# Optimization experiments

Hardware: AMD Instinct MI355X
Metric: run time of the kernel (lower is better)

## Reference

```python
import jax, jax.numpy as jnp
import numpy as np

N_EMBD = 384
NUM_HEADS = 6
HEAD_SIZE = 64


def setup_inputs() -> dict:
    key = jax.random.key(0)
    ks = jax.random.split(key, 6)
    B, T = 128, 256
    D = NUM_HEADS * HEAD_SIZE  # 384
    x = jax.random.normal(ks[0], (B, T, N_EMBD), dtype=jnp.float32)
    Wk = jax.random.normal(ks[1], (N_EMBD, D), dtype=jnp.float32) * (N_EMBD ** -0.5)
    Wq = jax.random.normal(ks[2], (N_EMBD, D), dtype=jnp.float32) * (N_EMBD ** -0.5)
    Wv = jax.random.normal(ks[3], (N_EMBD, D), dtype=jnp.float32) * (N_EMBD ** -0.5)
    Wp = jax.random.normal(ks[4], (D, N_EMBD), dtype=jnp.float32) * (D ** -0.5)
    bp = jax.random.normal(ks[5], (N_EMBD,), dtype=jnp.float32) * 0.01
    return {"x": x, "Wk": Wk, "Wq": Wq, "Wv": Wv, "Wp": Wp, "bp": bp}


def reference(x, Wk, Wq, Wv, Wp, bp):
    B, T, C = x.shape
    H, hs = NUM_HEADS, HEAD_SIZE
    # QKV projections -> [B, H, T, hs]
    q = (x @ Wq).reshape(B, T, H, hs).transpose(0, 2, 1, 3)
    k = (x @ Wk).reshape(B, T, H, hs).transpose(0, 2, 1, 3)
    v = (x @ Wv).reshape(B, T, H, hs).transpose(0, 2, 1, 3)
    # NOTE: original scales by C**-0.5 where C = n_embd (not head_size)
    scale = jnp.asarray(C, x.dtype) ** -0.5
    wei = jnp.einsum('bhtd,bhsd->bhts', q, k) * scale  # [B, H, T, T]
    causal = jnp.tril(jnp.ones((T, T), dtype=bool))
    wei = jnp.where(causal, wei, -jnp.inf)
    wei = jax.nn.softmax(wei, axis=-1)
    # dropout disabled (eval mode) for deterministic reference
    out = jnp.einsum('bhts,bhsd->bhtd', wei, v)  # [B, H, T, hs]
    out = out.transpose(0, 2, 1, 3).reshape(B, T, H * hs)
    return out @ Wp + bp
```

## Files before the change

kernel.cpp:

```cpp
#include <hip/hip_runtime.h>
#include <hip/hip_bf16.h>


#define T_SEQ 256
#define NH 6
#define HS 64
#define CIN 384
#define BATCH 128
#define BT (BATCH * T_SEQ)
#define ELEMS ((size_t)BT * CIN)

using f32x4  = __attribute__((ext_vector_type(4))) float;
using bf16x8 = __attribute__((ext_vector_type(8))) short;

typedef __attribute__((address_space(3))) void       lds_vp;
typedef __attribute__((address_space(1))) const void glob_vp;

static __device__ __forceinline__ unsigned short f2bf(float f) {
  union { float f; unsigned u; } v; v.f = f;
  unsigned r = v.u + 0x7FFFu + ((v.u >> 16) & 1u);
  return (unsigned short)(r >> 16);
}

static __device__ __forceinline__ bf16x8 ld_bf8(const unsigned short* p) {
  return *reinterpret_cast<const bf16x8*>(p);
}

static __device__ __forceinline__ void gl_lds16(const void* g, void* l) {
  __builtin_amdgcn_global_load_lds((glob_vp*)g, (lds_vp*)l, 16, 0, 0);
}

__global__ __launch_bounds__(256) void convert_x(
    const float* __restrict__ x, unsigned short* __restrict__ xb)
{
  size_t i = (((size_t)blockIdx.x << 8) + threadIdx.x) << 3;
  float4 f0 = *reinterpret_cast<const float4*>(x + i);
  float4 f1 = *reinterpret_cast<const float4*>(x + i + 4);
  uint4 pk;
  pk.x = f2bf(f0.x) | ((unsigned)f2bf(f0.y) << 16);
  pk.y = f2bf(f0.z) | ((unsigned)f2bf(f0.w) << 16);
  pk.z = f2bf(f1.x) | ((unsigned)f2bf(f1.y) << 16);
  pk.w = f2bf(f1.z) | ((unsigned)f2bf(f1.w) << 16);
  *reinterpret_cast<uint4*>(xb + i) = pk;
}

__global__ __launch_bounds__(256) void convert_wqkv(
    const float* __restrict__ Wq, const float* __restrict__ Wk,
    const float* __restrict__ Wv, unsigned short* __restrict__ dst)
{
  __shared__ float t[32][33];
  const int z = blockIdx.z;
  const float* __restrict__ W = (z == 0) ? Wq : (z == 1) ? Wk : Wv;
  const int tx = threadIdx.x & 31, ty = threadIdx.x >> 5;
  const int k0 = blockIdx.x * 32, n0 = blockIdx.y * 32;
#pragma unroll
  for (int i = 0; i < 4; ++i)
    t[ty + 8 * i][tx] = W[(size_t)(k0 + ty + 8 * i) * CIN + n0 + tx];
  __syncthreads();
#pragma unroll
  for (int i = 0; i < 4; ++i)
    dst[((size_t)z * CIN + n0 + ty + 8 * i) * CIN + k0 + tx] =
        f2bf(t[tx][ty + 8 * i]);
}

__global__ __launch_bounds__(256) void transpose_w(
    const float* __restrict__ W, unsigned short* __restrict__ dst)
{
  __shared__ float t[32][33];
  const int tx = threadIdx.x & 31, ty = threadIdx.x >> 5;
  const int k0 = blockIdx.x * 32, n0 = blockIdx.y * 32;
#pragma unroll
  for (int i = 0; i < 4; ++i)
    t[ty + 8 * i][tx] = W[(size_t)(k0 + ty + 8 * i) * CIN + n0 + tx];
  __syncthreads();
#pragma unroll
  for (int i = 0; i < 4; ++i)
    dst[((size_t)(n0 + ty + 8 * i)) * CIN + k0 + tx] = f2bf(t[tx][ty + 8 * i]);
}

__global__ __launch_bounds__(256) void gemm_qkv(
    const unsigned short* __restrict__ xb,
    const unsigned short* __restrict__ wt,
    unsigned short* __restrict__ q_ws, unsigned short* __restrict__ k_ws,
    unsigned short* __restrict__ vT_ws)
{
  __shared__ __align__(16) unsigned short XA[128][64];
  __shared__ __align__(16) unsigned short XB[128][64];

  const int tid = threadIdx.x;
  const int w = tid >> 6, l = tid & 63, g = l >> 4, c = l & 15;
  const int wr = w >> 1, wc = w & 1;

  const int wid = ((int)blockIdx.x & 7) * 288 + ((int)blockIdx.x >> 3);
  const int n_t = wid % 9, m_t = wid / 9;
  const int m0 = m_t * 128, n0 = n_t * 128;

  f32x4 acc[4][4];
#pragma unroll
  for (int mi = 0; mi < 4; ++mi)
#pragma unroll
    for (int nj = 0; nj < 4; ++nj) { f32x4 zz = {0.f,0.f,0.f,0.f}; acc[mi][nj] = zz; }

  const unsigned short* ga = xb + (size_t)(m0 + (w << 5) + (l >> 3)) * CIN + ((l & 7) << 3);
  const unsigned short* gb = wt + (size_t)(n0 + (w << 5) + (l >> 3)) * CIN + ((l & 7) << 3);
  char* lA = (char*)&XA[0][0] + (w << 12);
  char* lB = (char*)&XB[0][0] + (w << 12);

  for (int k0 = 0; k0 < CIN; k0 += 64) {
#pragma unroll
    for (int i = 0; i < 4; ++i) {
      gl_lds16(ga + k0 + i * 8 * CIN, lA + i * 1024);
      gl_lds16(gb + k0 + i * 8 * CIN, lB + i * 1024);
    }
    __syncthreads();
#pragma unroll
    for (int kk = 0; kk < 2; ++kk) {
      bf16x8 a[4], b[4];
#pragma unroll
      for (int mi = 0; mi < 4; ++mi)
        a[mi] = ld_bf8(&XA[wr * 64 + mi * 16 + c][kk * 32 + g * 8]);
#pragma unroll
      for (int nj = 0; nj < 4; ++nj)
        b[nj] = ld_bf8(&XB[wc * 64 + nj * 16 + c][kk * 32 + g * 8]);
#pragma unroll
      for (int mi = 0; mi < 4; ++mi)
#pragma unroll
        for (int nj = 0; nj < 4; ++nj)
          acc[mi][nj] = __builtin_amdgcn_mfma_f32_16x16x32_bf16(
              a[mi], b[nj], acc[mi][nj], 0, 0, 0);
    }
    __syncthreads();
  }

  const int z = n_t / 3;
  const int colw = (n_t % 3) * 128 + wc * 64;
#pragma unroll
  for (int nj = 0; nj < 4; ++nj) {
    const int cw = colw + nj * 16 + c;
    const int h = cw >> 6, d = cw & 63;
#pragma unroll
    for (int mi = 0; mi < 4; ++mi) {
      const int mrow = m0 + wr * 64 + mi * 16 + 4 * g;
      const int b = mrow >> 8, t0 = mrow & 255;
      if (z == 2) {
        ushort4 pk;
        pk.x = f2bf(acc[mi][nj][0]); pk.y = f2bf(acc[mi][nj][1]);
        pk.z = f2bf(acc[mi][nj][2]); pk.w = f2bf(acc[mi][nj][3]);
        *reinterpret_cast<ushort4*>(
            vT_ws + (((size_t)b * NH + h) * HS + d) * T_SEQ + t0) = pk;
      } else {
        unsigned short* dstb = (z == 0) ? q_ws : k_ws;
#pragma unroll
        for (int i = 0; i < 4; ++i)
          dstb[(((size_t)b * NH + h) * T_SEQ + t0 + i) * HS + d] =
              f2bf(acc[mi][nj][i]);
      }
    }
  }
}

template<int NT>
__device__ __forceinline__ void attn_tile(
    const unsigned short* __restrict__ qg,
    const unsigned short* KL, const unsigned short* VL,
    unsigned short* __restrict__ o_ws, int bh, int qt, int g, int c)
{
  const int q0 = qt * 16;
  const int kxor = (c & 7) << 4;

  const char* qrow = (const char*)qg + (size_t)(q0 + c) * 128;
  const bf16x8 qb0 = *reinterpret_cast<const bf16x8*>(qrow + g * 16);
  const bf16x8 qb1 = *reinterpret_cast<const bf16x8*>(qrow + 64 + g * 16);

  f32x4 s[NT];
#pragma unroll
  for (int kt = 0; kt < NT; ++kt) {
    const char* krow = (const char*)KL + (kt * 16 + c) * 128;
    bf16x8 ka0 = *reinterpret_cast<const bf16x8*>(krow + ((g * 16) ^ kxor));
    bf16x8 ka1 = *reinterpret_cast<const bf16x8*>(krow + ((64 + g * 16) ^ kxor));
    f32x4 z = {0.f, 0.f, 0.f, 0.f};
    z = __builtin_amdgcn_mfma_f32_16x16x32_bf16(ka0, qb0, z, 0, 0, 0);
    z = __builtin_amdgcn_mfma_f32_16x16x32_bf16(ka1, qb1, z, 0, 0, 0);
    s[kt] = z;
  }

  const float sc = 0.07362372251839260f;
  float mx = -1e30f;
#pragma unroll
  for (int kt = 0; kt < NT; ++kt)
#pragma unroll
    for (int i = 0; i < 4; ++i) {
      const int k = kt * 16 + 4 * g + i;
      float v = (k <= q0 + c) ? s[kt][i] * sc : -1e30f;
      s[kt][i] = v;
      mx = fmaxf(mx, v);
    }
  mx = fmaxf(mx, __shfl_xor(mx, 16));
  mx = fmaxf(mx, __shfl_xor(mx, 32));

  float sum = 0.f;
#pragma unroll
  for (int kt = 0; kt < NT; ++kt)
#pragma unroll
    for (int i = 0; i < 4; ++i) {
      float p = __builtin_exp2f(s[kt][i] - mx);
      s[kt][i] = p;
      sum += p;
    }
  sum += __shfl_xor(sum, 16);
  sum += __shfl_xor(sum, 32);
  const float inv = 1.0f / sum;

  unsigned pk0[NT], pk1[NT];
#pragma unroll
  for (int kt = 0; kt < NT; ++kt) {
    float2 p01 = {s[kt][0] * inv, s[kt][1] * inv};
    float2 p23 = {s[kt][2] * inv, s[kt][3] * inv};
    __hip_bfloat162 b01 = __float22bfloat162_rn(p01);
    __hip_bfloat162 b23 = __float22bfloat162_rn(p23);
    pk0[kt] = *reinterpret_cast<unsigned*>(&b01);
    pk1[kt] = *reinterpret_cast<unsigned*>(&b23);
  }

  f32x4 acc[4];
#pragma unroll
  for (int nt = 0; nt < 4; ++nt) { f32x4 zz = {0.f,0.f,0.f,0.f}; acc[nt] = zz; }

  const int srcA = ((g & 1) << 5) + c;
  const int srcB = srcA + 16;
  const bool hi = (g >= 2);
#pragma unroll
  for (int ks = 0; ks < NT / 2; ++ks) {
    unsigned a0A = __shfl(pk0[2 * ks],     srcA);
    unsigned a1A = __shfl(pk1[2 * ks],     srcA);
    unsigned a0B = __shfl(pk0[2 * ks],     srcB);
    unsigned a1B = __shfl(pk1[2 * ks],     srcB);
    unsigned b0A = __shfl(pk0[2 * ks + 1], srcA);
    unsigned b1A = __shfl(pk1[2 * ks + 1], srcA);
    unsigned b0B = __shfl(pk0[2 * ks + 1], srcB);
    unsigned b1B = __shfl(pk1[2 * ks + 1], srcB);
    union { unsigned u[4]; bf16x8 v; } pa;
    pa.u[0] = hi ? b0A : a0A;
    pa.u[1] = hi ? b1A : a1A;
    pa.u[2] = hi ? b0B : a0B;
    pa.u[3] = hi ? b1B : a1B;
#pragma unroll
    for (int nt = 0; nt < 4; ++nt) {
      const char* vrow = (const char*)VL + (nt * 16 + c) * 512;
      bf16x8 vb = *reinterpret_cast<const bf16x8*>(
          vrow + ((ks * 64 + g * 16) ^ kxor));
      acc[nt] = __builtin_amdgcn_mfma_f32_16x16x32_bf16(pa.v, vb, acc[nt], 0, 0, 0);
    }
  }

  const int b = bh / NH, h = bh % NH;
  unsigned short* ob = o_ws + ((size_t)(b * T_SEQ + q0)) * CIN + h * HS;
#pragma unroll
  for (int nt = 0; nt < 4; ++nt)
#pragma unroll
    for (int i = 0; i < 4; ++i)
      ob[(size_t)(4 * g + i) * CIN + nt * 16 + c] = f2bf(acc[nt][i]);
}

__global__ __launch_bounds__(512, 4) void attn_kernel(
    const unsigned short* __restrict__ q_ws,
    const unsigned short* __restrict__ k_ws,
    const unsigned short* __restrict__ vT_ws,
    unsigned short* __restrict__ o_ws)
{
  __shared__ __align__(16) unsigned short KL[256 * 64];
  __shared__ __align__(16) unsigned short VL[64 * 256];

  const int tid = threadIdx.x;
  const int w = tid >> 6, l = tid & 63, g = l >> 4, c = l & 15;
  const int bh = blockIdx.x;

  const char* kg = (const char*)(k_ws + (size_t)bh * T_SEQ * HS);
  const char* vg = (const char*)(vT_ws + (size_t)bh * HS * T_SEQ);
#pragma unroll
  for (int i = 0; i < 4; ++i) {
    const int cid = i * 512 + w * 64 + l;
    const int rk = cid >> 3, pk_ = cid & 7;
    gl_lds16(kg + rk * 128 + ((pk_ ^ (rk & 7)) << 4),
             (char*)KL + (size_t)(i * 512 + w * 64) * 16);
    const int rv = cid >> 5, pv = cid & 31;
    const int sv = (pv & ~7) | ((pv & 7) ^ (rv & 7));
    gl_lds16(vg + rv * 512 + (sv << 4),
             (char*)VL + (size_t)(i * 512 + w * 64) * 16);
  }
  __syncthreads();

  const unsigned short* qg = q_ws + (size_t)bh * T_SEQ * HS;
  switch (w) {
    case 0: attn_tile<2>(qg, KL, VL, o_ws, bh, 0, g, c);
            attn_tile<16>(qg, KL, VL, o_ws, bh, 15, g, c); break;
    case 1: attn_tile<2>(qg, KL, VL, o_ws, bh, 1, g, c);
            attn_tile<16>(qg, KL, VL, o_ws, bh, 14, g, c); break;
    case 2: attn_tile<4>(qg, KL, VL, o_ws, bh, 2, g, c);
            attn_tile<14>(qg, KL, VL, o_ws, bh, 13, g, c); break;
    case 3: attn_tile<4>(qg, KL, VL, o_ws, bh, 3, g, c);
            attn_tile<14>(qg, KL, VL, o_ws, bh, 12, g, c); break;
    case 4: attn_tile<6>(qg, KL, VL, o_ws, bh, 4, g, c);
            attn_tile<12>(qg, KL, VL, o_ws, bh, 11, g, c); break;
    case 5: attn_tile<6>(qg, KL, VL, o_ws, bh, 5, g, c);
            attn_tile<12>(qg, KL, VL, o_ws, bh, 10, g, c); break;
    case 6: attn_tile<8>(qg, KL, VL, o_ws, bh, 6, g, c);
            attn_tile<10>(qg, KL, VL, o_ws, bh, 9, g, c); break;
    case 7: attn_tile<8>(qg, KL, VL, o_ws, bh, 7, g, c);
            attn_tile<10>(qg, KL, VL, o_ws, bh, 8, g, c); break;
  }
}

__global__ __launch_bounds__(256) void proj_kernel(
    const unsigned short* __restrict__ ob,
    const unsigned short* __restrict__ wpt,
    const float* __restrict__ bp,
    float* __restrict__ out)
{
  __shared__ __align__(16) unsigned short XA[128][64];
  __shared__ __align__(16) unsigned short XB[128][64];

  const int tid = threadIdx.x;
  const int w = tid >> 6, l = tid & 63, g = l >> 4, c = l & 15;
  const int wr = w >> 1, wc = w & 1;

  const int wid = ((int)blockIdx.x & 7) * 96 + ((int)blockIdx.x >> 3);
  const int n_t = wid % 3, m_t = wid / 3;
  const int m0 = m_t * 128, n0 = n_t * 128;

  f32x4 acc[4][4];
#pragma unroll
  for (int mi = 0; mi < 4; ++mi)
#pragma unroll
    for (int nj = 0; nj < 4; ++nj) { f32x4 zz = {0.f,0.f,0.f,0.f}; acc[mi][nj] = zz; }

  const unsigned short* ga = ob  + (size_t)(m0 + (w << 5) + (l >> 3)) * CIN + ((l & 7) << 3);
  const unsigned short* gb = wpt + (size_t)(n0 + (w << 5) + (l >> 3)) * CIN + ((l & 7) << 3);
  char* lA = (char*)&XA[0][0] + (w << 12);
  char* lB = (char*)&XB[0][0] + (w << 12);

  for (int k0 = 0; k0 < CIN; k0 += 64) {
#pragma unroll
    for (int i = 0; i < 4; ++i) {
      gl_lds16(ga + k0 + i * 8 * CIN, lA + i * 1024);
      gl_lds16(gb + k0 + i * 8 * CIN, lB + i * 1024);
    }
    __syncthreads();
#pragma unroll
    for (int kk = 0; kk < 2; ++kk) {
      bf16x8 a[4], b[4];
#pragma unroll
      for (int mi = 0; mi < 4; ++mi)
        a[mi] = ld_bf8(&XA[wr * 64 + mi * 16 + c][kk * 32 + g * 8]);
#pragma unroll
      for (int nj = 0; nj < 4; ++nj)
        b[nj] = ld_bf8(&XB[wc * 64 + nj * 16 + c][kk * 32 + g * 8]);
#pragma unroll
      for (int mi = 0; mi < 4; ++mi)
#pragma unroll
        for (int nj = 0; nj < 4; ++nj)
          acc[mi][nj] = __builtin_amdgcn_mfma_f32_16x16x32_bf16(
              a[mi], b[nj], acc[mi][nj], 0, 0, 0);
    }
    __syncthreads();
  }

#pragma unroll
  for (int nj = 0; nj < 4; ++nj) {
    const int col = n0 + wc * 64 + nj * 16 + c;
    const float bias = bp[col];
#pragma unroll
    for (int mi = 0; mi < 4; ++mi) {
      const int mrow = m0 + wr * 64 + mi * 16 + 4 * g;
#pragma unroll
      for (int i = 0; i < 4; ++i)
        out[(size_t)(mrow + i) * CIN + col] = acc[mi][nj][i] + bias;
    }
  }
}

extern "C" void kernel_launch(void* const* d_in, const int* in_sizes, int n_in,
                              void* d_out, int out_size, void* d_ws, size_t ws_size,
                              hipStream_t stream)
{
  const float* x  = (const float*)d_in[0];
  const float* Wk = (const float*)d_in[1];
  const float* Wq = (const float*)d_in[2];
  const float* Wv = (const float*)d_in[3];
  const float* Wp = (const float*)d_in[4];
  const float* bp = (const float*)d_in[5];
  float* out = (float*)d_out;

  unsigned short* ws    = (unsigned short*)d_ws;
  unsigned short* xb_o  = ws;
  unsigned short* q_ws  = ws + ELEMS;
  unsigned short* k_ws  = ws + 2 * ELEMS;
  unsigned short* vT_ws = ws + 3 * ELEMS;
  unsigned short* wqkvT = (unsigned short*)d_out;

  convert_x   <<<6144, 256, 0, stream>>>(x, xb_o);
  convert_wqkv<<<dim3(12, 12, 3), 256, 0, stream>>>(Wq, Wk, Wv, wqkvT);
  gemm_qkv    <<<2304, 256, 0, stream>>>(xb_o, wqkvT, q_ws, k_ws, vT_ws);
  attn_kernel <<<BATCH * NH, 512, 0, stream>>>(q_ws, k_ws, vT_ws, xb_o);
  transpose_w <<<dim3(12, 12), 256, 0, stream>>>(Wp, q_ws);
  proj_kernel <<<768, 256, 0, stream>>>(xb_o, q_ws, bp, out);
}
```

Measured before the change: 130.1 us.

## Double-buffer GEMM LDS tiles with XOR swizzle and coalesce Q/K epilogue

Both the QKV and output-projection GEMMs now keep two LDS buffers, so the global-to-LDS load of the next K-slice is issued before the MFMAs on the current slice and overlaps with them. The LDS layout is XOR-swizzled by 16-byte chunks to avoid bank conflicts on the fragment reads. The Q/K epilogue stages results through LDS and writes each row as 16-byte coalesced stores instead of scattered 2-byte stores. Doubling LDS per block may reduce occupancy.

```diff
diff --git a/kernel.cpp b/kernel.cpp
--- a/kernel.cpp
+++ b/kernel.cpp
@@ -84,8 +84,8 @@
     unsigned short* __restrict__ q_ws, unsigned short* __restrict__ k_ws,
     unsigned short* __restrict__ vT_ws)
 {
-  __shared__ __align__(16) unsigned short XA[128][64];
-  __shared__ __align__(16) unsigned short XB[128][64];
+  __shared__ __align__(16) unsigned short XA[2][128][64];
+  __shared__ __align__(16) unsigned short XB[2][128][64];
 
   const int tid = threadIdx.x;
   const int w = tid >> 6, l = tid & 63, g = l >> 4, c = l & 15;
@@ -101,27 +101,43 @@
 #pragma unroll
     for (int nj = 0; nj < 4; ++nj) { f32x4 zz = {0.f,0.f,0.f,0.f}; acc[mi][nj] = zz; }
 
-  const unsigned short* ga = xb + (size_t)(m0 + (w << 5) + (l >> 3)) * CIN + ((l & 7) << 3);
-  const unsigned short* gb = wt + (size_t)(n0 + (w << 5) + (l >> 3)) * CIN + ((l & 7) << 3);
-  char* lA = (char*)&XA[0][0] + (w << 12);
-  char* lB = (char*)&XB[0][0] + (w << 12);
-
-  for (int k0 = 0; k0 < CIN; k0 += 64) {
-#pragma unroll
-    for (int i = 0; i < 4; ++i) {
-      gl_lds16(ga + k0 + i * 8 * CIN, lA + i * 1024);
-      gl_lds16(gb + k0 + i * 8 * CIN, lB + i * 1024);
-    }
-    __syncthreads();
+  const int lrow = l >> 3;
+  const int lchk = (l & 7) ^ lrow;
+  const char* ga = (const char*)xb +
+      ((size_t)(m0 + w * 32 + lrow) * CIN + lchk * 8) * 2;
+  const char* gb = (const char*)wt +
+      ((size_t)(n0 + w * 32 + lrow) * CIN + lchk * 8) * 2;
+
+#define STAGE_QKV(buf, k0)                                              \
+  {                                                                     \
+    _Pragma("unroll")                                                   \
+    for (int i_ = 0; i_ < 4; ++i_) {                                    \
+      gl_lds16(ga + ((k0) + i_ * 8 * CIN) * 2, &XA[buf][w * 32 + i_ * 8][0]); \
+      gl_lds16(gb + ((k0) + i_ * 8 * CIN) * 2, &XB[buf][w * 32 + i_ * 8][0]); \
+    }                                                                   \
+  }
+
+  STAGE_QKV(0, 0);
+  __syncthreads();
+
+  int cur = 0;
+  for (int t = 0; t < 6; ++t) {
+    if (t < 5) STAGE_QKV(cur ^ 1, (t + 1) * 64);
 #pragma unroll
     for (int kk = 0; kk < 2; ++kk) {
       bf16x8 a[4], b[4];
 #pragma unroll
-      for (int mi = 0; mi < 4; ++mi)
-        a[mi] = ld_bf8(&XA[wr * 64 + mi * 16 + c][kk * 32 + g * 8]);
-#pragma unroll
-      for (int nj = 0; nj < 4; ++nj)
-        b[nj] = ld_bf8(&XB[wc * 64 + nj * 16 + c][kk * 32 + g * 8]);
+      for (int mi = 0; mi < 4; ++mi) {
+        const int row = wr * 64 + mi * 16 + c;
+        a[mi] = *reinterpret_cast<const bf16x8*>(
+            (const char*)&XA[cur][row][0] + (((kk * 4 + g) ^ (c & 7)) << 4));
+      }
+#pragma unroll
+      for (int nj = 0; nj < 4; ++nj) {
+        const int row = wc * 64 + nj * 16 + c;
+        b[nj] = *reinterpret_cast<const bf16x8*>(
+            (const char*)&XB[cur][row][0] + (((kk * 4 + g) ^ (c & 7)) << 4));
+      }
 #pragma unroll
       for (int mi = 0; mi < 4; ++mi)
 #pragma unroll
@@ -130,33 +146,54 @@
               a[mi], b[nj], acc[mi][nj], 0, 0, 0);
     }
     __syncthreads();
+    cur ^= 1;
   }
 
   const int z = n_t / 3;
   const int colw = (n_t % 3) * 128 + wc * 64;
-#pragma unroll
-  for (int nj = 0; nj < 4; ++nj) {
-    const int cw = colw + nj * 16 + c;
-    const int h = cw >> 6, d = cw & 63;
-#pragma unroll
-    for (int mi = 0; mi < 4; ++mi) {
-      const int mrow = m0 + wr * 64 + mi * 16 + 4 * g;
-      const int b = mrow >> 8, t0 = mrow & 255;
-      if (z == 2) {
+  const int h = colw >> 6;
+  const int b = m0 >> 8;
+  const int trow0 = (m0 & 255) + wr * 64;
+
+  if (z == 2) {
+#pragma unroll
+    for (int nj = 0; nj < 4; ++nj) {
+      const int d = nj * 16 + c;
+#pragma unroll
+      for (int mi = 0; mi < 4; ++mi) {
+        const int t0 = trow0 + mi * 16 + 4 * g;
         ushort4 pk;
         pk.x = f2bf(acc[mi][nj][0]); pk.y = f2bf(acc[mi][nj][1]);
         pk.z = f2bf(acc[mi][nj][2]); pk.w = f2bf(acc[mi][nj][3]);
         *reinterpret_cast<ushort4*>(
             vT_ws + (((size_t)b * NH + h) * HS + d) * T_SEQ + t0) = pk;
-      } else {
-        unsigned short* dstb = (z == 0) ? q_ws : k_ws;
-#pragma unroll
-        for (int i = 0; i < 4; ++i)
-          dstb[(((size_t)b * NH + h) * T_SEQ + t0 + i) * HS + d] =
-              f2bf(acc[mi][nj][i]);
       }
     }
-  }
+  } else {
+    unsigned short* dstb = (z == 0) ? q_ws : k_ws;
+    char* OS = (char*)XA + w * 8192;
+#pragma unroll
+    for (int nj = 0; nj < 4; ++nj)
+#pragma unroll
+      for (int mi = 0; mi < 4; ++mi)
+#pragma unroll
+        for (int i = 0; i < 4; ++i) {
+          const int r = mi * 16 + 4 * g + i;
+          const int chk = (nj * 2 + (c >> 3)) ^ (r & 7);
+          *reinterpret_cast<unsigned short*>(
+              OS + r * 128 + (chk << 4) + (c & 7) * 2) = f2bf(acc[mi][nj][i]);
+        }
+    __syncthreads();
+    unsigned short* gdst = dstb + (((size_t)b * NH + h) * T_SEQ + trow0) * HS;
+#pragma unroll
+    for (int p = 0; p < 8; ++p) {
+      const int r = p * 8 + (l >> 3);
+      const int chk = (l & 7) ^ (r & 7);
+      uint4 v = *reinterpret_cast<const uint4*>(OS + r * 128 + (chk << 4));
+      *reinterpret_cast<uint4*>((char*)gdst + r * 128 + (l & 7) * 16) = v;
+    }
+  }
+#undef STAGE_QKV
 }
 
 template<int NT>
@@ -317,8 +354,8 @@
     const float* __restrict__ bp,
     float* __restrict__ out)
 {
-  __shared__ __align__(16) unsigned short XA[128][64];
-  __shared__ __align__(16) unsigned short XB[128][64];
+  __shared__ __align__(16) unsigned short XA[2][128][64];
+  __shared__ __align__(16) unsigned short XB[2][128][64];
 
   const int tid = threadIdx.x;
   const int w = tid >> 6, l = tid & 63, g = l >> 4, c = l & 15;
@@ -334,27 +371,43 @@
 #pragma unroll
     for (int nj = 0; nj < 4; ++nj) { f32x4 zz = {0.f,0.f,0.f,0.f}; acc[mi][nj] = zz; }
 
-  const unsigned short* ga = ob  + (size_t)(m0 + (w << 5) + (l >> 3)) * CIN + ((l & 7) << 3);
-  const unsigned short* gb = wpt + (size_t)(n0 + (w << 5) + (l >> 3)) * CIN + ((l & 7) << 3);
-  char* lA = (char*)&XA[0][0] + (w << 12);
-  char* lB = (char*)&XB[0][0] + (w << 12);
-
-  for (int k0 = 0; k0 < CIN; k0 += 64) {
-#pragma unroll
-    for (int i = 0; i < 4; ++i) {
-      gl_lds16(ga + k0 + i * 8 * CIN, lA + i * 1024);
-      gl_lds16(gb + k0 + i * 8 * CIN, lB + i * 1024);
-    }
-    __syncthreads();
+  const int lrow = l >> 3;
+  const int lchk = (l & 7) ^ lrow;
+  const char* ga = (const char*)ob +
+      ((size_t)(m0 + w * 32 + lrow) * CIN + lchk * 8) * 2;
+  const char* gb = (const char*)wpt +
+      ((size_t)(n0 + w * 32 + lrow) * CIN + lchk * 8) * 2;
+
+#define STAGE_PRJ(buf, k0)                                              \
+  {                                                                     \
+    _Pragma("unroll")                                                   \
+    for (int i_ = 0; i_ < 4; ++i_) {                                    \
+      gl_lds16(ga + ((k0) + i_ * 8 * CIN) * 2, &XA[buf][w * 32 + i_ * 8][0]); \
+      gl_lds16(gb + ((k0) + i_ * 8 * CIN) * 2, &XB[buf][w * 32 + i_ * 8][0]); \
+    }                                                                   \
+  }
+
+  STAGE_PRJ(0, 0);
+  __syncthreads();
+
+  int cur = 0;
+  for (int t = 0; t < 6; ++t) {
+    if (t < 5) STAGE_PRJ(cur ^ 1, (t + 1) * 64);
 #pragma unroll
     for (int kk = 0; kk < 2; ++kk) {
       bf16x8 a[4], b[4];
 #pragma unroll
-      for (int mi = 0; mi < 4; ++mi)
-        a[mi] = ld_bf8(&XA[wr * 64 + mi * 16 + c][kk * 32 + g * 8]);
-#pragma unroll
-      for (int nj = 0; nj < 4; ++nj)
-        b[nj] = ld_bf8(&XB[wc * 64 + nj * 16 + c][kk * 32 + g * 8]);
+      for (int mi = 0; mi < 4; ++mi) {
+        const int row = wr * 64 + mi * 16 + c;
+        a[mi] = *reinterpret_cast<const bf16x8*>(
+            (const char*)&XA[cur][row][0] + (((kk * 4 + g) ^ (c & 7)) << 4));
+      }
+#pragma unroll
+      for (int nj = 0; nj < 4; ++nj) {
+        const int row = wc * 64 + nj * 16 + c;
+        b[nj] = *reinterpret_cast<const bf16x8*>(
+            (const char*)&XB[cur][row][0] + (((kk * 4 + g) ^ (c & 7)) << 4));
+      }
 #pragma unroll
       for (int mi = 0; mi < 4; ++mi)
 #pragma unroll
@@ -363,6 +416,7 @@
               a[mi], b[nj], acc[mi][nj], 0, 0, 0);
     }
     __syncthreads();
+    cur ^= 1;
   }
 
 #pragma unroll
@@ -377,6 +431,7 @@
         out[(size_t)(mrow + i) * CIN + col] = acc[mi][nj][i] + bias;
     }
   }
+#undef STAGE_PRJ
 }
 
 extern "C" void kernel_launch(void* const* d_in, const int* in_sizes, int n_in,
```

Measured after the change: 119.9 us. 7.8% less time.
